# Kernel optimization log

Hardware: AMD Instinct MI355X
Metric: run time of the kernel (lower is better)

The kernel has to match this reference:

```python
import jax, jax.numpy as jnp
import numpy as np

ROPE_BASE = 10000.0

def _rope_cos_sin(T, dh, dtype):
    inv_freq = 1.0 / (ROPE_BASE ** (jnp.arange(0, dh, 2, dtype=jnp.float32) / dh))
    t = jnp.arange(T, dtype=jnp.float32)
    freqs = jnp.outer(t, inv_freq)                      # [T, dh/2]
    emb = jnp.concatenate([freqs, freqs], axis=-1)      # [T, dh]
    return jnp.cos(emb).astype(dtype), jnp.sin(emb).astype(dtype)

def _rotate_half(x):
    x1, x2 = jnp.split(x, 2, axis=-1)
    return jnp.concatenate([-x2, x1], axis=-1)

def setup_inputs() -> dict:
    key = jax.random.key(0)
    k1, k2, k3 = jax.random.split(key, 3)
    B, T, D = 2, 2048, 2048
    x = jax.random.normal(k1, (B, T, D), dtype=jnp.float32)
    w_qkv = jax.random.normal(k2, (3 * D, D), dtype=jnp.float32) * (D ** -0.5)
    w_proj = jax.random.normal(k3, (D, D), dtype=jnp.float32) * (D ** -0.5)
    return {"x": x, "w_qkv": w_qkv, "w_proj": w_proj}

def reference(x, w_qkv, w_proj):
    B, T, D = x.shape
    H = 16
    Dh = D // H
    scale = Dh ** -0.5
    qkv = x @ w_qkv.T                                   # [B,T,3D]
    qkv = qkv.reshape(B, T, 3, H, Dh).transpose(2, 0, 3, 1, 4)  # [3,B,H,T,Dh]
    q, k, v = qkv[0], qkv[1], qkv[2]
    cos, sin = _rope_cos_sin(T, Dh, x.dtype)            # [T,Dh] each, offset=0
    q = q * cos + _rotate_half(q) * sin
    k = k * cos + _rotate_half(k) * sin
    attn = jnp.einsum('bhqd,bhkd->bhqk', q, k) * scale  # [B,H,T,T]
    causal = jnp.triu(jnp.full((T, T), -jnp.inf, dtype=attn.dtype), k=1)
    attn = jax.nn.softmax(attn + causal, axis=-1)
    out = jnp.einsum('bhqk,bhkd->bhqd', attn, v)        # [B,H,T,Dh]
    out = out.transpose(0, 2, 1, 3).reshape(B, T, D)
    return out @ w_proj.T
```

## Files before the change

kernel.cpp:

```cpp
#include <hip/hip_runtime.h>
#include <stdint.h>

typedef unsigned short u16;
typedef unsigned int   u32;
typedef __attribute__((ext_vector_type(8))) __bf16 bf16x8;
typedef __attribute__((ext_vector_type(4))) float  f32x4;

#define MFMA_16x16x32_BF16(a, b, c) __builtin_amdgcn_mfma_f32_16x16x32_bf16((a), (b), (c), 0, 0, 0)

__device__ __forceinline__ u16 f2b(float f) {
    u32 u = __builtin_bit_cast(u32, f);
    u32 r = (u + 0x7FFFu + ((u >> 16) & 1u)) >> 16;
    return (u16)r;
}
__device__ __forceinline__ float b2f(u16 h) {
    u32 u = ((u32)h) << 16;
    return __builtin_bit_cast(float, u);
}

__device__ __forceinline__ void gload_lds16(const void* g, void* l) {
    __builtin_amdgcn_global_load_lds(
        (const __attribute__((address_space(1))) u32*)g,
        (__attribute__((address_space(3))) u32*)l,
        16, 0, 0);
}

__global__ __launch_bounds__(256) void cast3(const float* __restrict__ x,
                                             const float* __restrict__ wq,
                                             const float* __restrict__ wp,
                                             u16* __restrict__ xb,
                                             u16* __restrict__ wqb,
                                             u16* __restrict__ wpb) {
    const int n1 = 8388608, n2 = 12582912, n3 = 4194304;
    const int total4 = (n1 + n2 + n3) / 4;
    for (int i = blockIdx.x * blockDim.x + threadIdx.x; i < total4;
         i += gridDim.x * blockDim.x) {
        int e = i * 4;
        const float* src; u16* dst; int off;
        if (e < n1)            { src = x;  dst = xb;  off = e; }
        else if (e < n1 + n2)  { src = wq; dst = wqb; off = e - n1; }
        else                   { src = wp; dst = wpb; off = e - n1 - n2; }
        float4 v = *(const float4*)(src + off);
        ushort4 o;
        o.x = f2b(v.x); o.y = f2b(v.y); o.z = f2b(v.z); o.w = f2b(v.w);
        *(ushort4*)(dst + off) = o;
    }
}

template <int OUT_BF16>
__global__ __launch_bounds__(256) void gemm_bt(const u16* __restrict__ A,
                                               const u16* __restrict__ Bt,
                                               void* __restrict__ Cout,
                                               int M, int N, int K) {
    __shared__ u16 Al[128 * 64];
    __shared__ u16 Bl[128 * 64];
    const int tid  = threadIdx.x;
    const int w    = tid >> 6;
    const int lane = tid & 63;
    const int quad = lane >> 4;
    const int l16  = lane & 15;
    const int m0 = blockIdx.y * 128;
    const int n0 = blockIdx.x * 128;
    const int wm = (w >> 1) * 64;
    const int wn = (w & 1) * 64;

    f32x4 acc[4][4];
#pragma unroll
    for (int i = 0; i < 4; i++) {
#pragma unroll
        for (int j = 0; j < 4; j++) acc[i][j] = (f32x4){0.f, 0.f, 0.f, 0.f};
    }

    const int srow = tid >> 3;
    const int scol = ((tid & 7) ^ (srow & 7)) * 8;
    const u16* Abase = A + (size_t)(m0 + srow) * K + scol;
    const u16* Bbase = Bt + (size_t)(n0 + srow) * K + scol;
    char* AlB = (char*)Al + w * 1024;
    char* BlB = (char*)Bl + w * 1024;
    const int fx = (l16 & 7);

    for (int k0 = 0; k0 < K; k0 += 64) {
        __syncthreads();
#pragma unroll
        for (int i = 0; i < 4; i++) {
            gload_lds16(Abase + (size_t)i * 32 * K + k0, AlB + i * 4096);
            gload_lds16(Bbase + (size_t)i * 32 * K + k0, BlB + i * 4096);
        }
        __syncthreads();
#pragma unroll
        for (int ks = 0; ks < 2; ks++) {
            const int cb = ((ks * 4 + quad) ^ fx) * 8;
            bf16x8 Af[4];
#pragma unroll
            for (int mi = 0; mi < 4; mi++)
                Af[mi] = *(const bf16x8*)&Al[(wm + mi * 16 + l16) * 64 + cb];
#pragma unroll
            for (int ni = 0; ni < 4; ni++) {
                bf16x8 Bf = *(const bf16x8*)&Bl[(wn + ni * 16 + l16) * 64 + cb];
#pragma unroll
                for (int mi = 0; mi < 4; mi++)
                    acc[mi][ni] = MFMA_16x16x32_BF16(Af[mi], Bf, acc[mi][ni]);
            }
        }
    }

    const int row0 = m0 + wm + quad * 4;
    const int col0 = n0 + wn + l16;
#pragma unroll
    for (int mi = 0; mi < 4; mi++) {
#pragma unroll
        for (int r = 0; r < 4; r++) {
            size_t rowb = (size_t)(row0 + mi * 16 + r) * N;
#pragma unroll
            for (int ni = 0; ni < 4; ni++) {
                float v = acc[mi][ni][r];
                if (OUT_BF16) ((u16*)Cout)[rowb + col0 + ni * 16] = f2b(v);
                else          ((float*)Cout)[rowb + col0 + ni * 16] = v;
            }
        }
    }
}

__global__ __launch_bounds__(256) void rope_qk(const u16* __restrict__ qkv,
                                               u16* __restrict__ Q,
                                               u16* __restrict__ K) {
    const int bt = blockIdx.x;
    const int b = bt >> 11, t = bt & 2047;
    const u16* row = qkv + (size_t)bt * 6144;
    const int tid = threadIdx.x;

#pragma unroll
    for (int it = 0; it < 8; it++) {
        int p   = it * 256 + tid;
        int qk  = p >> 10;
        int rem = p & 1023;
        int h   = rem >> 6;
        int i   = rem & 63;
        float x1 = b2f(row[qk * 2048 + h * 128 + i]);
        float x2 = b2f(row[qk * 2048 + h * 128 + i + 64]);
        float inv = expf(-0.14391156f * (float)i);
        float th  = (float)t * inv;
        float s, c;
        sincosf(th, &s, &c);
        float o1 = x1 * c - x2 * s;
        float o2 = x2 * c + x1 * s;
        u16* dst = (qk ? K : Q) + ((size_t)((b * 16 + h) * 2048 + t)) * 128;
        dst[i]      = f2b(o1);
        dst[i + 64] = f2b(o2);
    }
}

__global__ __launch_bounds__(256) void vtrans(const u16* __restrict__ qkv,
                                              u16* __restrict__ VT) {
    __shared__ u16 S[64 * 136];
    const int tc = blockIdx.x;
    const int bh = blockIdx.y;
    const int b = bh >> 4, h = bh & 15;
    const int tid = threadIdx.x;

#pragma unroll
    for (int i = 0; i < 4; i++) {
        int idx = i * 256 + tid;
        int t  = idx >> 4;
        int d8 = (idx & 15) * 8;
        uint4 v = *(const uint4*)(qkv + ((size_t)(b * 2048 + tc * 64 + t)) * 6144
                                      + 4096 + h * 128 + d8);
        *(uint4*)&S[t * 136 + d8] = v;
    }
    __syncthreads();
#pragma unroll
    for (int i = 0; i < 4; i++) {
        int idx = i * 256 + tid;
        int d  = idx >> 3;
        int t8 = (idx & 7) * 8;
        u16 tmp[8];
#pragma unroll
        for (int j = 0; j < 8; j++) tmp[j] = S[(t8 + j) * 136 + d];
        *(uint4*)(VT + ((size_t)(bh * 128 + d)) * 2048 + tc * 64 + t8) = *(uint4*)tmp;
    }
}

__global__ __launch_bounds__(256) void attn(const u16* __restrict__ Q,
                                            const u16* __restrict__ Kg,
                                            const u16* __restrict__ VTg,
                                            u16* __restrict__ O) {
    __shared__ u16 Kl[2][64 * 128];
    __shared__ u16 Vt[2][128 * 64];
    __shared__ u16 Pl[4 * 16 * 76];

    const int tid  = threadIdx.x;
    const int w    = tid >> 6;
    const int lane = tid & 63;
    const int quad = lane >> 4;
    const int l16  = lane & 15;
    const int pair = blockIdx.x;
    const int bh   = blockIdx.y;
    const int b = bh >> 4, h = bh & 15;
    const size_t base = (size_t)bh * 2048 * 128;
    const u16* Qb  = Q + base;
    const u16* Kb  = Kg + base;
    const u16* VTb = VTg + base;
    u16* Plw = Pl + w * 16 * 76;
    const float scale = 0.08838834764831845f;

    const int krow = tid >> 4;
    const int kcol = (((tid & 15) ^ (krow & 7)) * 8);
    const int vrow = w * 8 + (lane >> 3);
    const int vcol = (((lane & 7) ^ (vrow & 7)) * 8);
    const int fx   = (l16 & 7);

    for (int s = 0; s < 2; s++) {
        const int qt   = s ? (31 - pair) : pair;
        const int q0   = qt * 64;
        const int row0 = q0 + w * 16;

        bf16x8 Qf[4];
#pragma unroll
        for (int kk = 0; kk < 4; kk++)
            Qf[kk] = *(const bf16x8*)&Qb[(size_t)(row0 + l16) * 128 + kk * 32 + quad * 8];

        f32x4 Oacc[8];
#pragma unroll
        for (int ni = 0; ni < 8; ni++) Oacc[ni] = (f32x4){0.f, 0.f, 0.f, 0.f};
        float mrow = -1e30f, lrow = 0.f;

        const int nkt = qt + 1;

        __syncthreads();
        {
            const u16* ksrc = Kb + (size_t)krow * 128 + kcol;
            char* kdst = (char*)Kl[0] + w * 1024;
            const u16* vsrc = VTb + (size_t)vrow * 2048 + vcol;
            char* vdst = (char*)Vt[0] + w * 1024;
#pragma unroll
            for (int i = 0; i < 4; i++) {
                gload_lds16(ksrc + (size_t)i * 16 * 128, kdst + i * 4096);
                gload_lds16(vsrc + (size_t)i * 32 * 2048, vdst + i * 4096);
            }
        }

        for (int kt = 0; kt < nkt; kt++) {
            const int kt0 = kt * 64;
            const int cur = kt & 1;
            __syncthreads();

            if (kt + 1 < nkt) {
                const int kt1 = kt0 + 64;
                const u16* ksrc = Kb + (size_t)(kt1 + krow) * 128 + kcol;
                char* kdst = (char*)Kl[cur ^ 1] + w * 1024;
                const u16* vsrc = VTb + (size_t)vrow * 2048 + kt1 + vcol;
                char* vdst = (char*)Vt[cur ^ 1] + w * 1024;
#pragma unroll
                for (int i = 0; i < 4; i++) {
                    gload_lds16(ksrc + (size_t)i * 16 * 128, kdst + i * 4096);
                    gload_lds16(vsrc + (size_t)i * 32 * 2048, vdst + i * 4096);
                }
            }

            const u16* Klc = Kl[cur];
            const u16* Vtc = Vt[cur];

            f32x4 ST[4];
#pragma unroll
            for (int mi = 0; mi < 4; mi++) ST[mi] = (f32x4){0.f, 0.f, 0.f, 0.f};
#pragma unroll
            for (int kk = 0; kk < 4; kk++) {
                const int cb = ((kk * 4 + quad) ^ fx) * 8;
#pragma unroll
                for (int mi = 0; mi < 4; mi++) {
                    bf16x8 Kf = *(const bf16x8*)&Klc[(mi * 16 + l16) * 128 + cb];
                    ST[mi] = MFMA_16x16x32_BF16(Kf, Qf[kk], ST[mi]);
                }
            }

            const bool needs_mask = (kt0 + 63) > row0;
            const int qg = row0 + l16;
            float tmax = -1e30f;
#pragma unroll
            for (int mi = 0; mi < 4; mi++) {
#pragma unroll
                for (int r = 0; r < 4; r++) {
                    float sv = ST[mi][r] * scale;
                    if (needs_mask) {
                        int kg = kt0 + mi * 16 + quad * 4 + r;
                        sv = (kg > qg) ? -1e30f : sv;
                    }
                    ST[mi][r] = sv;
                    tmax = fmaxf(tmax, sv);
                }
            }
            tmax = fmaxf(tmax, __shfl_xor(tmax, 16));
            tmax = fmaxf(tmax, __shfl_xor(tmax, 32));

            float mnew  = fmaxf(mrow, tmax);
            float alpha = __expf(mrow - mnew);
            mrow = mnew;

            float tsum = 0.f;
#pragma unroll
            for (int mi = 0; mi < 4; mi++) {
#pragma unroll
                for (int r = 0; r < 4; r++) {
                    float p = __expf(ST[mi][r] - mnew);
                    ST[mi][r] = p;
                    tsum += p;
                }
            }
            lrow = lrow * alpha + tsum;

#pragma unroll
            for (int mi = 0; mi < 4; mi++) {
                ushort4 pk;
                pk.x = f2b(ST[mi][0]); pk.y = f2b(ST[mi][1]);
                pk.z = f2b(ST[mi][2]); pk.w = f2b(ST[mi][3]);
                *(ushort4*)&Plw[l16 * 76 + mi * 16 + quad * 4] = pk;
            }

            float aRow[4];
#pragma unroll
            for (int r = 0; r < 4; r++) aRow[r] = __shfl(alpha, quad * 4 + r);
#pragma unroll
            for (int ni = 0; ni < 8; ni++) {
#pragma unroll
                for (int r = 0; r < 4; r++) Oacc[ni][r] *= aRow[r];
            }

            bf16x8 Pf[2];
#pragma unroll
            for (int kk = 0; kk < 2; kk++)
                Pf[kk] = *(const bf16x8*)&Plw[l16 * 76 + kk * 32 + quad * 8];
#pragma unroll
            for (int kk = 0; kk < 2; kk++) {
                const int cb = ((kk * 4 + quad) ^ fx) * 8;
#pragma unroll
                for (int ni = 0; ni < 8; ni++) {
                    bf16x8 Vf = *(const bf16x8*)&Vtc[(ni * 16 + l16) * 64 + cb];
                    Oacc[ni] = MFMA_16x16x32_BF16(Pf[kk], Vf, Oacc[ni]);
                }
            }
        }

        lrow += __shfl_xor(lrow, 16);
        lrow += __shfl_xor(lrow, 32);
        float inv = 1.0f / lrow;
        float iRow[4];
#pragma unroll
        for (int r = 0; r < 4; r++) iRow[r] = __shfl(inv, quad * 4 + r);

#pragma unroll
        for (int r = 0; r < 4; r++) {
            int t = row0 + quad * 4 + r;
            size_t rowb = ((size_t)(b * 2048 + t)) * 2048 + (size_t)(h * 128);
#pragma unroll
            for (int ni = 0; ni < 8; ni++)
                O[rowb + ni * 16 + l16] = f2b(Oacc[ni][r] * iRow[r]);
        }
    }
}

extern "C" void kernel_launch(void* const* d_in, const int* in_sizes, int n_in,
                              void* d_out, int out_size, void* d_ws, size_t ws_size,
                              hipStream_t stream) {
    const float* x  = (const float*)d_in[0];
    const float* wq = (const float*)d_in[1];
    const float* wp = (const float*)d_in[2];

    char* ws = (char*)d_ws;
    u16* xb   = (u16*)(ws + 0);
    u16* wqb  = (u16*)(ws + 16777216);
    u16* wpb  = (u16*)(ws + 41943040);
    u16* qkvb = (u16*)(ws + 50331648);
    u16* Qr   = (u16*)(ws + 100663296);
    u16* Kr   = (u16*)(ws + 117440512);
    u16* VTt  = (u16*)(ws + 134217728);
    u16* Ob   = (u16*)(ws + 50331648);
    if (ws_size < 150994944) return;

    cast3<<<2048, 256, 0, stream>>>(x, wq, wp, xb, wqb, wpb);
    gemm_bt<1><<<dim3(48, 32), 256, 0, stream>>>(xb, wqb, qkvb, 4096, 6144, 2048);
    rope_qk<<<4096, 256, 0, stream>>>(qkvb, Qr, Kr);
    vtrans<<<dim3(32, 32), 256, 0, stream>>>(qkvb, VTt);
    attn<<<dim3(16, 32), 256, 0, stream>>>(Qr, Kr, VTt, Ob);
    gemm_bt<0><<<dim3(16, 32), 256, 0, stream>>>(Ob, wpb, (float*)d_out, 4096, 2048, 2048);
}
```

Before: 408.6 us.

## Add 256x256-tile pipelined GEMM for QKV projection with XCD-aware block swizzle

Adds a new 512-thread GEMM kernel using 256x256 output tiles, double-buffered LDS staging via direct global-to-LDS loads, split K-halves interleaved with MFMA phases, priority hints, and an XCD-aware block index swizzle. It is used for the QKV projection when 128KB of dynamic shared memory can be enabled, with a fallback to the old 128-tile kernel. The aim is more operand reuse per tile and better overlap of loads with matrix math. In exchange it uses large LDS per block (limiting occupancy) and launches only 384 blocks, which risks wave quantization.

```diff
diff --git a/kernel.cpp b/kernel.cpp
--- a/kernel.cpp
+++ b/kernel.cpp
@@ -121,6 +121,139 @@
     }
 }
 
+template <int OUT_BF16>
+__global__ __launch_bounds__(512, 2) void gemm256(const u16* __restrict__ A,
+                                                  const u16* __restrict__ Bt,
+                                                  void* __restrict__ Cout,
+                                                  int N, int K, int nbx) {
+    extern __shared__ char smem[];
+    const int tid  = threadIdx.x;
+    const int w    = tid >> 6;
+    const int lane = tid & 63;
+    const int quad = lane >> 4;
+    const int l16  = lane & 15;
+
+    const int nwg = gridDim.x;
+    const int cpx = nwg >> 3;
+    const int bid = blockIdx.x;
+    const int swz = (bid & 7) * cpx + (bid >> 3);
+    const int bx  = swz % nbx;
+    const int by  = swz / nbx;
+    const int m0 = by * 256, n0 = bx * 256;
+    const int wr = w >> 2, wc = w & 3;
+
+    const int loff = (((l16 >> 3) * 32) + quad * 8 + (l16 & 7)) * 16;
+
+    const int rowS = ((tid >> 5) * 8) + (tid & 7);
+    const int kbS  = (tid >> 3) & 3;
+    const u16* Asrc = A  + (size_t)(m0 + rowS) * K + kbS * 8;
+    const u16* Bsrc = Bt + (size_t)(n0 + rowS) * K + kbS * 8;
+    char* const smA = smem;
+    char* const smB = smem + 65536;
+    const int woff = w * 1024;
+
+    f32x4 acc[8][4];
+#pragma unroll
+    for (int i = 0; i < 8; i++)
+#pragma unroll
+        for (int j = 0; j < 4; j++) acc[i][j] = (f32x4){0.f, 0.f, 0.f, 0.f};
+
+    const int NT = K >> 6;
+
+#define STAGE_UNIT(t_, kh_, isB_)                                              \
+    {                                                                          \
+        const u16* s_ = (isB_ ? Bsrc : Asrc) + (size_t)(t_)*64 + (kh_)*32;     \
+        char* d_ = (isB_ ? smB : smA) + ((t_)&1) * 32768 + (kh_)*16384 + woff; \
+        gload_lds16(s_, d_);                                                   \
+        gload_lds16(s_ + (size_t)128 * K, d_ + 8192);                          \
+    }
+
+#define LOAD_A(KH, MH)                                                         \
+    {                                                                          \
+        const char* Ab_ = smA + bufo + (KH)*16384 + (wr * 128 + (MH)*64) * 64; \
+        _Pragma("unroll")                                                      \
+        for (int mi = 0; mi < 4; mi++)                                         \
+            Af[mi] = *(const bf16x8*)(Ab_ + mi * 1024 + loff);                 \
+    }
+
+#define LOAD_B(KH)                                                             \
+    {                                                                          \
+        const char* Bb_ = smB + bufo + (KH)*16384 + (wc * 64) * 64;            \
+        _Pragma("unroll")                                                      \
+        for (int ni = 0; ni < 4; ni++)                                         \
+            Bf[ni] = *(const bf16x8*)(Bb_ + ni * 1024 + loff);                 \
+    }
+
+#define MFMA_PHASE(MB)                                                         \
+    __builtin_amdgcn_s_setprio(1);                                             \
+    _Pragma("unroll")                                                          \
+    for (int ni = 0; ni < 4; ni++) {                                           \
+        _Pragma("unroll")                                                      \
+        for (int mi = 0; mi < 4; mi++)                                         \
+            acc[(MB) + mi][ni] =                                               \
+                MFMA_16x16x32_BF16(Af[mi], Bf[ni], acc[(MB) + mi][ni]);        \
+    }                                                                          \
+    __builtin_amdgcn_s_setprio(0);                                             \
+    __builtin_amdgcn_sched_barrier(0);
+
+    STAGE_UNIT(0, 0, 0);
+    STAGE_UNIT(0, 0, 1);
+    STAGE_UNIT(0, 1, 0);
+    STAGE_UNIT(0, 1, 1);
+
+    for (int t = 0; t < NT; ++t) {
+        const int bufo = (t & 1) * 32768;
+        const int pf = (t + 1 < NT);
+        bf16x8 Af[4], Bf[4];
+
+        asm volatile("s_waitcnt vmcnt(4)" ::: "memory");
+        __builtin_amdgcn_s_barrier();
+        LOAD_A(0, 0);
+        LOAD_B(0);
+        if (pf) STAGE_UNIT(t + 1, 0, 0);
+        MFMA_PHASE(0);
+
+        __builtin_amdgcn_s_barrier();
+        LOAD_A(0, 1);
+        if (pf) STAGE_UNIT(t + 1, 0, 1);
+        MFMA_PHASE(4);
+
+        if (pf) { asm volatile("s_waitcnt vmcnt(4)" ::: "memory"); }
+        else    { asm volatile("s_waitcnt vmcnt(0)" ::: "memory"); }
+        __builtin_amdgcn_s_barrier();
+        LOAD_A(1, 0);
+        LOAD_B(1);
+        if (pf) STAGE_UNIT(t + 1, 1, 0);
+        MFMA_PHASE(0);
+
+        __builtin_amdgcn_s_barrier();
+        LOAD_A(1, 1);
+        if (pf) STAGE_UNIT(t + 1, 1, 1);
+        MFMA_PHASE(4);
+    }
+
+#undef STAGE_UNIT
+#undef LOAD_A
+#undef LOAD_B
+#undef MFMA_PHASE
+
+    const int row0 = m0 + wr * 128 + quad * 4;
+    const int col0 = n0 + wc * 64 + l16;
+#pragma unroll
+    for (int mf = 0; mf < 8; mf++) {
+#pragma unroll
+        for (int r = 0; r < 4; r++) {
+            size_t rowb = (size_t)(row0 + mf * 16 + r) * N;
+#pragma unroll
+            for (int ni = 0; ni < 4; ni++) {
+                float v = acc[mf][ni][r];
+                if (OUT_BF16) ((u16*)Cout)[rowb + col0 + ni * 16] = f2b(v);
+                else          ((float*)Cout)[rowb + col0 + ni * 16] = v;
+            }
+        }
+    }
+}
+
 __global__ __launch_bounds__(256) void rope_qk(const u16* __restrict__ qkv,
                                                u16* __restrict__ Q,
                                                u16* __restrict__ K) {
@@ -376,8 +509,20 @@
     u16* Ob   = (u16*)(ws + 50331648);
     if (ws_size < 150994944) return;
 
+    static int use256 = -1;
+    if (use256 < 0) {
+        hipError_t e = hipFuncSetAttribute(
+            reinterpret_cast<const void*>(&gemm256<1>),
+            hipFuncAttributeMaxDynamicSharedMemorySize, 131072);
+        use256 = (e == hipSuccess) ? 1 : 0;
+    }
+
     cast3<<<2048, 256, 0, stream>>>(x, wq, wp, xb, wqb, wpb);
-    gemm_bt<1><<<dim3(48, 32), 256, 0, stream>>>(xb, wqb, qkvb, 4096, 6144, 2048);
+    if (use256) {
+        gemm256<1><<<384, 512, 131072, stream>>>(xb, wqb, qkvb, 6144, 2048, 24);
+    } else {
+        gemm_bt<1><<<dim3(48, 32), 256, 0, stream>>>(xb, wqb, qkvb, 4096, 6144, 2048);
+    }
     rope_qk<<<4096, 256, 0, stream>>>(qkvb, Qr, Kr);
     vtrans<<<dim3(32, 32), 256, 0, stream>>>(qkvb, VTt);
     attn<<<dim3(16, 32), 256, 0, stream>>>(Qr, Kr, VTt, Ob);
```

Measured after the change: 421.2 us. 3.1% more time.

## Use two-wave attention blocks with 32 query rows per wave and lazy rescale

Applied to the files above, without the earlier changes.

The attention kernel drops to 128 threads per block, and each wave now owns two 16-row query tiles. Every K and V fragment read from LDS therefore feeds two MFMAs, halving LDS traffic per unit of compute, at the cost of more registers and fewer waves to hide latency. The online-softmax rescale of the output accumulator now runs only when a row maximum grows by more than 8, skipping most rescales. The rope kernel computes the sin/cos table once per block in shared memory instead of per element.

```diff
diff --git a/kernel.cpp b/kernel.cpp
--- a/kernel.cpp
+++ b/kernel.cpp
@@ -124,10 +124,19 @@
 __global__ __launch_bounds__(256) void rope_qk(const u16* __restrict__ qkv,
                                                u16* __restrict__ Q,
                                                u16* __restrict__ K) {
+    __shared__ float cs[64], sn[64];
     const int bt = blockIdx.x;
     const int b = bt >> 11, t = bt & 2047;
     const u16* row = qkv + (size_t)bt * 6144;
     const int tid = threadIdx.x;
+
+    if (tid < 64) {
+        float inv = __expf(-0.14391156f * (float)tid);
+        float s, c;
+        sincosf((float)t * inv, &s, &c);
+        sn[tid] = s; cs[tid] = c;
+    }
+    __syncthreads();
 
 #pragma unroll
     for (int it = 0; it < 8; it++) {
@@ -138,10 +147,7 @@
         int i   = rem & 63;
         float x1 = b2f(row[qk * 2048 + h * 128 + i]);
         float x2 = b2f(row[qk * 2048 + h * 128 + i + 64]);
-        float inv = expf(-0.14391156f * (float)i);
-        float th  = (float)t * inv;
-        float s, c;
-        sincosf(th, &s, &c);
+        float s = sn[i], c = cs[i];
         float o1 = x1 * c - x2 * s;
         float o2 = x2 * c + x1 * s;
         u16* dst = (qk ? K : Q) + ((size_t)((b * 16 + h) * 2048 + t)) * 128;
@@ -180,13 +186,13 @@
     }
 }
 
-__global__ __launch_bounds__(256) void attn(const u16* __restrict__ Q,
-                                            const u16* __restrict__ Kg,
-                                            const u16* __restrict__ VTg,
-                                            u16* __restrict__ O) {
+__global__ __launch_bounds__(128, 1) void attn(const u16* __restrict__ Q,
+                                               const u16* __restrict__ Kg,
+                                               const u16* __restrict__ VTg,
+                                               u16* __restrict__ O) {
     __shared__ u16 Kl[2][64 * 128];
     __shared__ u16 Vt[2][128 * 64];
-    __shared__ u16 Pl[4 * 16 * 76];
+    __shared__ u16 Pl[2 * 32 * 76];
 
     const int tid  = threadIdx.x;
     const int w    = tid >> 6;
@@ -200,29 +206,35 @@
     const u16* Qb  = Q + base;
     const u16* Kb  = Kg + base;
     const u16* VTb = VTg + base;
-    u16* Plw = Pl + w * 16 * 76;
+    u16* Plw = Pl + w * 32 * 76;
     const float scale = 0.08838834764831845f;
 
     const int krow = tid >> 4;
-    const int kcol = (((tid & 15) ^ (krow & 7)) * 8);
-    const int vrow = w * 8 + (lane >> 3);
-    const int vcol = (((lane & 7) ^ (vrow & 7)) * 8);
+    const int kcol = ((tid & 15) ^ (krow & 7)) * 8;
+    const int vrow = tid >> 3;
+    const int vcol = ((tid & 7) ^ (vrow & 7)) * 8;
     const int fx   = (l16 & 7);
 
     for (int s = 0; s < 2; s++) {
         const int qt   = s ? (31 - pair) : pair;
         const int q0   = qt * 64;
-        const int row0 = q0 + w * 16;
-
-        bf16x8 Qf[4];
+        const int row0 = q0 + w * 32;
+
+        bf16x8 Qf[4][2];
 #pragma unroll
         for (int kk = 0; kk < 4; kk++)
-            Qf[kk] = *(const bf16x8*)&Qb[(size_t)(row0 + l16) * 128 + kk * 32 + quad * 8];
-
-        f32x4 Oacc[8];
-#pragma unroll
-        for (int ni = 0; ni < 8; ni++) Oacc[ni] = (f32x4){0.f, 0.f, 0.f, 0.f};
-        float mrow = -1e30f, lrow = 0.f;
+#pragma unroll
+            for (int qi = 0; qi < 2; qi++)
+                Qf[kk][qi] = *(const bf16x8*)
+                    &Qb[(size_t)(row0 + qi * 16 + l16) * 128 + kk * 32 + quad * 8];
+
+        f32x4 Oacc[8][2];
+#pragma unroll
+        for (int ni = 0; ni < 8; ni++)
+#pragma unroll
+            for (int qi = 0; qi < 2; qi++) Oacc[ni][qi] = (f32x4){0.f, 0.f, 0.f, 0.f};
+        float m[2]    = {-1e30f, -1e30f};
+        float lsum[2] = {0.f, 0.f};
 
         const int nkt = qt + 1;
 
@@ -233,9 +245,9 @@
             const u16* vsrc = VTb + (size_t)vrow * 2048 + vcol;
             char* vdst = (char*)Vt[0] + w * 1024;
 #pragma unroll
-            for (int i = 0; i < 4; i++) {
-                gload_lds16(ksrc + (size_t)i * 16 * 128, kdst + i * 4096);
-                gload_lds16(vsrc + (size_t)i * 32 * 2048, vdst + i * 4096);
+            for (int i = 0; i < 8; i++) {
+                gload_lds16(ksrc + (size_t)i * 1024, kdst + i * 2048);
+                gload_lds16(vsrc + (size_t)i * 16 * 2048, vdst + i * 2048);
             }
         }
 
@@ -251,109 +263,128 @@
                 const u16* vsrc = VTb + (size_t)vrow * 2048 + kt1 + vcol;
                 char* vdst = (char*)Vt[cur ^ 1] + w * 1024;
 #pragma unroll
-                for (int i = 0; i < 4; i++) {
-                    gload_lds16(ksrc + (size_t)i * 16 * 128, kdst + i * 4096);
-                    gload_lds16(vsrc + (size_t)i * 32 * 2048, vdst + i * 4096);
+                for (int i = 0; i < 8; i++) {
+                    gload_lds16(ksrc + (size_t)i * 1024, kdst + i * 2048);
+                    gload_lds16(vsrc + (size_t)i * 16 * 2048, vdst + i * 2048);
                 }
             }
 
             const u16* Klc = Kl[cur];
             const u16* Vtc = Vt[cur];
 
-            f32x4 ST[4];
-#pragma unroll
-            for (int mi = 0; mi < 4; mi++) ST[mi] = (f32x4){0.f, 0.f, 0.f, 0.f};
+            f32x4 ST[4][2];
+#pragma unroll
+            for (int mi = 0; mi < 4; mi++)
+#pragma unroll
+                for (int qi = 0; qi < 2; qi++) ST[mi][qi] = (f32x4){0.f, 0.f, 0.f, 0.f};
 #pragma unroll
             for (int kk = 0; kk < 4; kk++) {
                 const int cb = ((kk * 4 + quad) ^ fx) * 8;
 #pragma unroll
                 for (int mi = 0; mi < 4; mi++) {
                     bf16x8 Kf = *(const bf16x8*)&Klc[(mi * 16 + l16) * 128 + cb];
-                    ST[mi] = MFMA_16x16x32_BF16(Kf, Qf[kk], ST[mi]);
-                }
-            }
-
-            const bool needs_mask = (kt0 + 63) > row0;
-            const int qg = row0 + l16;
-            float tmax = -1e30f;
-#pragma unroll
-            for (int mi = 0; mi < 4; mi++) {
-#pragma unroll
-                for (int r = 0; r < 4; r++) {
-                    float sv = ST[mi][r] * scale;
-                    if (needs_mask) {
-                        int kg = kt0 + mi * 16 + quad * 4 + r;
-                        sv = (kg > qg) ? -1e30f : sv;
+                    ST[mi][0] = MFMA_16x16x32_BF16(Kf, Qf[kk][0], ST[mi][0]);
+                    ST[mi][1] = MFMA_16x16x32_BF16(Kf, Qf[kk][1], ST[mi][1]);
+                }
+            }
+
+            float tmax[2] = {-1e30f, -1e30f};
+#pragma unroll
+            for (int qi = 0; qi < 2; qi++) {
+                const bool needs_mask = (kt0 + 63) > (row0 + qi * 16);
+                const int qg = row0 + qi * 16 + l16;
+#pragma unroll
+                for (int mi = 0; mi < 4; mi++) {
+#pragma unroll
+                    for (int r = 0; r < 4; r++) {
+                        float sv = ST[mi][qi][r] * scale;
+                        if (needs_mask) {
+                            int kg = kt0 + mi * 16 + quad * 4 + r;
+                            sv = (kg > qg) ? -1e30f : sv;
+                        }
+                        ST[mi][qi][r] = sv;
+                        tmax[qi] = fmaxf(tmax[qi], sv);
                     }
-                    ST[mi][r] = sv;
-                    tmax = fmaxf(tmax, sv);
-                }
-            }
-            tmax = fmaxf(tmax, __shfl_xor(tmax, 16));
-            tmax = fmaxf(tmax, __shfl_xor(tmax, 32));
-
-            float mnew  = fmaxf(mrow, tmax);
-            float alpha = __expf(mrow - mnew);
-            mrow = mnew;
-
-            float tsum = 0.f;
-#pragma unroll
-            for (int mi = 0; mi < 4; mi++) {
-#pragma unroll
-                for (int r = 0; r < 4; r++) {
-                    float p = __expf(ST[mi][r] - mnew);
-                    ST[mi][r] = p;
-                    tsum += p;
-                }
-            }
-            lrow = lrow * alpha + tsum;
-
-#pragma unroll
-            for (int mi = 0; mi < 4; mi++) {
-                ushort4 pk;
-                pk.x = f2b(ST[mi][0]); pk.y = f2b(ST[mi][1]);
-                pk.z = f2b(ST[mi][2]); pk.w = f2b(ST[mi][3]);
-                *(ushort4*)&Plw[l16 * 76 + mi * 16 + quad * 4] = pk;
-            }
-
-            float aRow[4];
-#pragma unroll
-            for (int r = 0; r < 4; r++) aRow[r] = __shfl(alpha, quad * 4 + r);
-#pragma unroll
-            for (int ni = 0; ni < 8; ni++) {
-#pragma unroll
-                for (int r = 0; r < 4; r++) Oacc[ni][r] *= aRow[r];
-            }
-
-            bf16x8 Pf[2];
+                }
+                tmax[qi] = fmaxf(tmax[qi], __shfl_xor(tmax[qi], 16));
+                tmax[qi] = fmaxf(tmax[qi], __shfl_xor(tmax[qi], 32));
+            }
+
+            if (__any((tmax[0] > m[0] + 8.0f) || (tmax[1] > m[1] + 8.0f))) {
+#pragma unroll
+                for (int qi = 0; qi < 2; qi++) {
+                    float mnew  = fmaxf(m[qi], tmax[qi]);
+                    float alpha = __expf(m[qi] - mnew);
+                    m[qi] = mnew;
+                    lsum[qi] *= alpha;
+                    float aRow[4];
+#pragma unroll
+                    for (int r = 0; r < 4; r++) aRow[r] = __shfl(alpha, quad * 4 + r);
+#pragma unroll
+                    for (int ni = 0; ni < 8; ni++)
+#pragma unroll
+                        for (int r = 0; r < 4; r++) Oacc[ni][qi][r] *= aRow[r];
+                }
+            }
+
+#pragma unroll
+            for (int qi = 0; qi < 2; qi++) {
+                float ts = 0.f;
+#pragma unroll
+                for (int mi = 0; mi < 4; mi++) {
+#pragma unroll
+                    for (int r = 0; r < 4; r++) {
+                        float p = __expf(ST[mi][qi][r] - m[qi]);
+                        ST[mi][qi][r] = p;
+                        ts += p;
+                    }
+                }
+                lsum[qi] += ts;
+#pragma unroll
+                for (int mi = 0; mi < 4; mi++) {
+                    ushort4 pk;
+                    pk.x = f2b(ST[mi][qi][0]); pk.y = f2b(ST[mi][qi][1]);
+                    pk.z = f2b(ST[mi][qi][2]); pk.w = f2b(ST[mi][qi][3]);
+                    *(ushort4*)&Plw[(qi * 16 + l16) * 76 + mi * 16 + quad * 4] = pk;
+                }
+            }
+
+            bf16x8 Pf[2][2];
 #pragma unroll
             for (int kk = 0; kk < 2; kk++)
-                Pf[kk] = *(const bf16x8*)&Plw[l16 * 76 + kk * 32 + quad * 8];
+#pragma unroll
+                for (int qi = 0; qi < 2; qi++)
+                    Pf[kk][qi] = *(const bf16x8*)
+                        &Plw[(qi * 16 + l16) * 76 + kk * 32 + quad * 8];
 #pragma unroll
             for (int kk = 0; kk < 2; kk++) {
                 const int cb = ((kk * 4 + quad) ^ fx) * 8;
 #pragma unroll
                 for (int ni = 0; ni < 8; ni++) {
                     bf16x8 Vf = *(const bf16x8*)&Vtc[(ni * 16 + l16) * 64 + cb];
-                    Oacc[ni] = MFMA_16x16x32_BF16(Pf[kk], Vf, Oacc[ni]);
-                }
-            }
-        }
-
-        lrow += __shfl_xor(lrow, 16);
-        lrow += __shfl_xor(lrow, 32);
-        float inv = 1.0f / lrow;
-        float iRow[4];
-#pragma unroll
-        for (int r = 0; r < 4; r++) iRow[r] = __shfl(inv, quad * 4 + r);
-
-#pragma unroll
-        for (int r = 0; r < 4; r++) {
-            int t = row0 + quad * 4 + r;
-            size_t rowb = ((size_t)(b * 2048 + t)) * 2048 + (size_t)(h * 128);
-#pragma unroll
-            for (int ni = 0; ni < 8; ni++)
-                O[rowb + ni * 16 + l16] = f2b(Oacc[ni][r] * iRow[r]);
+                    Oacc[ni][0] = MFMA_16x16x32_BF16(Pf[kk][0], Vf, Oacc[ni][0]);
+                    Oacc[ni][1] = MFMA_16x16x32_BF16(Pf[kk][1], Vf, Oacc[ni][1]);
+                }
+            }
+        }
+
+#pragma unroll
+        for (int qi = 0; qi < 2; qi++) {
+            float l2 = lsum[qi];
+            l2 += __shfl_xor(l2, 16);
+            l2 += __shfl_xor(l2, 32);
+            float inv = 1.0f / l2;
+            float iRow[4];
+#pragma unroll
+            for (int r = 0; r < 4; r++) iRow[r] = __shfl(inv, quad * 4 + r);
+#pragma unroll
+            for (int r = 0; r < 4; r++) {
+                int t = row0 + qi * 16 + quad * 4 + r;
+                size_t rowb = ((size_t)(b * 2048 + t)) * 2048 + (size_t)(h * 128);
+#pragma unroll
+                for (int ni = 0; ni < 8; ni++)
+                    O[rowb + ni * 16 + l16] = f2b(Oacc[ni][qi][r] * iRow[r]);
+            }
         }
     }
 }
@@ -380,6 +411,6 @@
     gemm_bt<1><<<dim3(48, 32), 256, 0, stream>>>(xb, wqb, qkvb, 4096, 6144, 2048);
     rope_qk<<<4096, 256, 0, stream>>>(qkvb, Qr, Kr);
     vtrans<<<dim3(32, 32), 256, 0, stream>>>(qkvb, VTt);
-    attn<<<dim3(16, 32), 256, 0, stream>>>(Qr, Kr, VTt, Ob);
+    attn<<<dim3(16, 32), 128, 0, stream>>>(Qr, Kr, VTt, Ob);
     gemm_bt<0><<<dim3(16, 32), 256, 0, stream>>>(Ob, wpb, (float*)d_out, 4096, 2048, 2048);
 }
```

After: 411.1 us. No clear change (+0.6%).
